# Performance work log

Measured on AMD Instinct MI355X. Metric: run time of the kernel, lower is better.

Reference implementation:

```python
import jax, jax.numpy as jnp
import numpy as np

N = 50000      # total nodes
C = 128        # in_channels
G = 4          # num_groups
B = 50         # number of graphs
NPG = N // B   # nodes per graph = 1000
E = 250000     # total edges (intra-graph)
COUT = 128     # conv out_channels


def setup_inputs() -> dict:
    key = jax.random.key(0)
    ks = jax.random.split(key, 6)
    sc = 1.0 / np.sqrt(C)
    x = jax.random.normal(ks[0], (N, C), dtype=jnp.float32)
    W_group = jax.random.normal(ks[1], (C, G), dtype=jnp.float32) * sc
    W_self = jax.random.normal(ks[2], (C, COUT), dtype=jnp.float32) * sc
    W_nbr = jax.random.normal(ks[3], (C, COUT), dtype=jnp.float32) * sc
    b = jnp.zeros((COUT,), dtype=jnp.float32)
    # intra-graph edges: E//B edges per graph, endpoints offset by graph id
    epg = E // B
    offs = (jnp.arange(E, dtype=jnp.int32) // epg) * NPG
    src = offs + jax.random.randint(ks[4], (E,), 0, NPG, dtype=jnp.int32)
    dst = offs + jax.random.randint(ks[5], (E,), 0, NPG, dtype=jnp.int32)
    edge_index = jnp.stack([src, dst])
    batch = (jnp.arange(N, dtype=jnp.int32) // NPG)
    # expanded node e = i*G*NPG + g*NPG + j maps back to original node i*NPG + j
    eidx = jnp.arange(G * N, dtype=jnp.int32)
    group_ptr = (eidx // (G * NPG)) * NPG + (eidx % NPG)
    return dict(x=x, W_group=W_group, W_self=W_self, W_nbr=W_nbr, b=b,
                edge_index=edge_index, batch=batch, group_ptr=group_ptr)


def reference(x, W_group, W_self, W_nbr, b, edge_index, batch, group_ptr):
    # soft group assignment: s = softmax(x @ W_group).T -> [G, N]
    s = jax.nn.softmax(x @ W_group, axis=-1).T
    # outer-product expansion: [G, N, C]
    ex = s[:, :, None] * x[None, :, :]
    # per-graph cat ordering: (g, graph i, local j) -> i*G*NPG + g*NPG + j
    ex = ex.reshape(G, B, NPG, C).transpose(1, 0, 2, 3).reshape(G * N, C)
    # expanded adjacency: replicate each graph's edges once per group
    src, dst = edge_index[0], edge_index[1]
    goff = jnp.arange(G, dtype=src.dtype)[:, None] * NPG            # [G, 1]
    src_exp = ((src // NPG) * (G * NPG))[None, :] + goff + (src % NPG)[None, :]
    dst_exp = ((dst // NPG) * (G * NPG))[None, :] + goff + (dst % NPG)[None, :]
    src_exp = src_exp.reshape(-1)
    dst_exp = dst_exp.reshape(-1)
    # GraphConv on expanded graph: self transform + sum-aggregated neighbor transform
    msg = (ex @ W_nbr)[src_exp]                                      # [G*E, COUT]
    agg = jax.ops.segment_sum(msg, dst_exp, num_segments=G * N)
    out = ex @ W_self + agg + b                                      # [G*N, COUT]
    # scatter-reduce G group copies back onto N original nodes
    return jax.ops.segment_sum(out, group_ptr, num_segments=N)
```

## Files before the change

kernel.cpp:

```cpp
#include <hip/hip_runtime.h>

constexpr int N_NODES  = 50000;
constexpr int C_IN     = 128;
constexpr int C_OUT    = 128;
constexpr int E_EDGES  = 250000;
constexpr int G_GRP    = 4;
constexpr int TM       = 32;
constexpr int CAP      = 32;
constexpr int NXCD     = 8;


typedef __attribute__((ext_vector_type(8))) short     short8;
typedef __attribute__((ext_vector_type(4))) float     f32x4;
typedef __attribute__((ext_vector_type(2))) unsigned  u32x2;

__device__ __forceinline__ unsigned short f2bf(float f) {
    unsigned u = __builtin_bit_cast(unsigned, f);
    u += 0x7fffu + ((u >> 16) & 1u);
    return (unsigned short)(u >> 16);
}
__device__ __forceinline__ unsigned pack2(float lo, float hi) {
    return (unsigned)f2bf(lo) | ((unsigned)f2bf(hi) << 16);
}

__device__ __forceinline__ int xcd_swizzle(int bid, int nblocks) {
    int q = nblocks / NXCD, r = nblocks % NXCD;
    int xcd = bid % NXCD, lid = bid / NXCD;
    return (xcd < r ? xcd * (q + 1) : r * (q + 1) + (xcd - r) * q) + lid;
}

constexpr int EDGE_BLOCKS  = (E_EDGES + 255) / 256;
constexpr int WPREP_BLOCKS = (C_OUT * 256) / 256;

__global__ __launch_bounds__(256) void fill_prep_kernel(
    const int* __restrict__ src, const int* __restrict__ dst,
    int* __restrict__ cnt, int* __restrict__ buckets,
    const float* __restrict__ Wself, const float* __restrict__ Wnbr,
    unsigned short* __restrict__ WT)
{
    int b = blockIdx.x;
    if (b < EDGE_BLOCKS) {
        int e = b * 256 + threadIdx.x;
        if (e < E_EDGES) {
            int d = dst[e];
            int pos = atomicAdd(&cnt[d], 1);
            if (pos < CAP) buckets[(size_t)d * CAP + pos] = src[e];
        }
    } else {
        int idx = (b - EDGE_BLOCKS) * 256 + threadIdx.x;
        int c = idx >> 8, k = idx & 255;
        float v = (k < 128) ? Wself[k * C_OUT + c] : Wnbr[(k - 128) * C_OUT + c];
        WT[idx] = f2bf(v);
    }
}

constexpr int GATHER_BLOCKS = N_NODES / 8;

__global__ __launch_bounds__(256) void gather_kernel(
    const float* __restrict__ x,
    const int* __restrict__ cnt,
    const int* __restrict__ buckets,
    unsigned short* __restrict__ xa_bf)
{
    int wg   = xcd_swizzle(blockIdx.x, GATHER_BLOCKS);
    int tid  = threadIdx.x;
    int n    = wg * 8 + (tid >> 5);
    int q    = tid & 31;

    const float4* x4 = reinterpret_cast<const float4*>(x);
    int d = cnt[n];
    if (d > CAP) d = CAP;
    const int* sp = buckets + (size_t)n * CAP;

    float ax = 0.f, ay = 0.f, az = 0.f, aw = 0.f;
    int e = 0;
    for (; e + 4 <= d; e += 4) {
        int s0 = sp[e], s1 = sp[e + 1], s2 = sp[e + 2], s3 = sp[e + 3];
        float4 v0 = x4[(size_t)s0 * 32 + q];
        float4 v1 = x4[(size_t)s1 * 32 + q];
        float4 v2 = x4[(size_t)s2 * 32 + q];
        float4 v3 = x4[(size_t)s3 * 32 + q];
        ax += (v0.x + v1.x) + (v2.x + v3.x);
        ay += (v0.y + v1.y) + (v2.y + v3.y);
        az += (v0.z + v1.z) + (v2.z + v3.z);
        aw += (v0.w + v1.w) + (v2.w + v3.w);
    }
    for (; e < d; ++e) {
        int s = sp[e];
        float4 v = x4[(size_t)s * 32 + q];
        ax += v.x; ay += v.y; az += v.z; aw += v.w;
    }

    u32x2 pk{pack2(ax, ay), pack2(az, aw)};
    *reinterpret_cast<u32x2*>(&xa_bf[(size_t)n * 128 + q * 4]) = pk;
}

constexpr int GEMM_BLOCKS = (N_NODES + TM - 1) / TM;

__global__ __launch_bounds__(256) void mfma_gemm_kernel(
    const float* __restrict__ x,
    const unsigned short* __restrict__ xa_bf,
    const unsigned short* __restrict__ WT,
    const float* __restrict__ bias,
    float* __restrict__ out)
{
    __shared__ unsigned char Ab[TM * 512];

    int wg = xcd_swizzle(blockIdx.x, GEMM_BLOCKS);
    const int tid  = threadIdx.x;
    const int row0 = wg * TM;

    #pragma unroll
    for (int i = 0; i < 4; ++i) {
        int idx = tid + i * 256;
        int r = idx >> 5, q = idx & 31;
        int n = row0 + r;
        float4 v = make_float4(0.f, 0.f, 0.f, 0.f);
        if (n < N_NODES) v = reinterpret_cast<const float4*>(x)[(size_t)n * 32 + q];
        unsigned lo = pack2(v.x, v.y), hi = pack2(v.z, v.w);
        int byte = (r * 512 + q * 8) ^ ((r & 7) << 4);
        *reinterpret_cast<u32x2*>(&Ab[byte]) = u32x2{lo, hi};
    }

    #pragma unroll
    for (int i = 0; i < 4; ++i) {
        int idx = tid + i * 256;
        int r = idx >> 5, q = idx & 31;
        int n = row0 + r;
        u32x2 pk{0u, 0u};
        if (n < N_NODES)
            pk = *reinterpret_cast<const u32x2*>(&xa_bf[(size_t)n * 128 + q * 4]);
        int byte = (r * 512 + 256 + q * 8) ^ ((r & 7) << 4);
        *reinterpret_cast<u32x2*>(&Ab[byte]) = pk;
    }
    __syncthreads();

    const int lane = tid & 63;
    const int w    = tid >> 6;
    const int rt   = w >> 1;
    const int ct0  = (w & 1) * 4;

    short8 a[8];
    {
        int r  = rt * 16 + (lane & 15);
        int kb = (lane >> 4) * 16;
        #pragma unroll
        for (int ks = 0; ks < 8; ++ks) {
            int byte = (r * 512 + ks * 64 + kb) ^ ((r & 7) << 4);
            a[ks] = *reinterpret_cast<const short8*>(&Ab[byte]);
        }
    }

    #pragma unroll
    for (int cti = 0; cti < 4; ++cti) {
        int ct = ct0 + cti;
        int c  = ct * 16 + (lane & 15);
        const short8* bp = reinterpret_cast<const short8*>(WT + (size_t)c * 256)
                           + (lane >> 4);
        f32x4 acc = {0.f, 0.f, 0.f, 0.f};
        #pragma unroll
        for (int ks = 0; ks < 8; ++ks) {
            short8 b = bp[ks * 4];
            acc = __builtin_amdgcn_mfma_f32_16x16x32_bf16(a[ks], b, acc, 0, 0, 0);
        }
        float bv = (float)G_GRP * bias[c];
        #pragma unroll
        for (int i = 0; i < 4; ++i) {
            int rr = row0 + rt * 16 + (lane >> 4) * 4 + i;
            if (rr < N_NODES) out[(size_t)rr * C_OUT + c] = acc[i] + bv;
        }
    }
}

extern "C" void kernel_launch(void* const* d_in, const int* in_sizes, int n_in,
                              void* d_out, int out_size, void* d_ws, size_t ws_size,
                              hipStream_t stream)
{
    const float* x     = (const float*)d_in[0];
    const float* Wself = (const float*)d_in[2];
    const float* Wnbr  = (const float*)d_in[3];
    const float* bias  = (const float*)d_in[4];
    const int*   eidx  = (const int*)d_in[5];

    const int* src = eidx;
    const int* dst = eidx + E_EDGES;

    int* cnt     = (int*)d_ws;
    int* buckets = cnt + N_NODES;
    unsigned short* WT    = (unsigned short*)(buckets + (size_t)N_NODES * CAP);
    unsigned short* xa_bf = WT + (size_t)C_OUT * 256;

    float* out = (float*)d_out;

    hipMemsetAsync(cnt, 0, (size_t)N_NODES * sizeof(int), stream);

    fill_prep_kernel<<<EDGE_BLOCKS + WPREP_BLOCKS, 256, 0, stream>>>(
        src, dst, cnt, buckets, Wself, Wnbr, WT);

    gather_kernel<<<GATHER_BLOCKS, 256, 0, stream>>>(x, cnt, buckets, xa_bf);

    mfma_gemm_kernel<<<GEMM_BLOCKS, 256, 0, stream>>>(
        x, xa_bf, WT, bias, out);
}
```

Measured before the change: 67.38 us.

## Replace bucket build and gather with per-graph LDS atomic scatter, enlarge GEMM tiles

```diff
diff --git a/kernel.cpp b/kernel.cpp
--- a/kernel.cpp
+++ b/kernel.cpp
@@ -5,9 +5,9 @@
 constexpr int C_OUT    = 128;
 constexpr int E_EDGES  = 250000;
 constexpr int G_GRP    = 4;
-constexpr int TM       = 32;
-constexpr int CAP      = 32;
-constexpr int NXCD     = 8;
+constexpr int NPG      = 1000;
+constexpr int EPG      = 5000;
+constexpr int B_GRAPHS = 50;
 
 
 typedef __attribute__((ext_vector_type(8))) short     short8;
@@ -23,108 +23,103 @@
     return (unsigned)f2bf(lo) | ((unsigned)f2bf(hi) << 16);
 }
 
-__device__ __forceinline__ int xcd_swizzle(int bid, int nblocks) {
-    int q = nblocks / NXCD, r = nblocks % NXCD;
-    int xcd = bid % NXCD, lid = bid / NXCD;
-    return (xcd < r ? xcd * (q + 1) : r * (q + 1) + (xcd - r) * q) + lid;
-}
+constexpr int SCATTER_BLOCKS = B_GRAPHS * 4;
+constexpr int WPREP_BLOCKS   = (C_OUT * 256) / 512;
 
-constexpr int EDGE_BLOCKS  = (E_EDGES + 255) / 256;
-constexpr int WPREP_BLOCKS = (C_OUT * 256) / 256;
+__global__ __launch_bounds__(512) void scatter_prep_kernel(
+    const float* __restrict__ x,
+    const int* __restrict__ src, const int* __restrict__ dst,
+    const float* __restrict__ Wself, const float* __restrict__ Wnbr,
+    unsigned short* __restrict__ WT, unsigned short* __restrict__ xa_bf)
+{
+    __shared__ float acc[NPG * 32];
 
-__global__ __launch_bounds__(256) void fill_prep_kernel(
-    const int* __restrict__ src, const int* __restrict__ dst,
-    int* __restrict__ cnt, int* __restrict__ buckets,
-    const float* __restrict__ Wself, const float* __restrict__ Wnbr,
-    unsigned short* __restrict__ WT)
-{
-    int b = blockIdx.x;
-    if (b < EDGE_BLOCKS) {
-        int e = b * 256 + threadIdx.x;
-        if (e < E_EDGES) {
-            int d = dst[e];
-            int pos = atomicAdd(&cnt[d], 1);
-            if (pos < CAP) buckets[(size_t)d * CAP + pos] = src[e];
-        }
-    } else {
-        int idx = (b - EDGE_BLOCKS) * 256 + threadIdx.x;
+    const int b   = blockIdx.x;
+    const int tid = threadIdx.x;
+
+    if (b >= SCATTER_BLOCKS) {
+        int idx = (b - SCATTER_BLOCKS) * 512 + tid;
         int c = idx >> 8, k = idx & 255;
         float v = (k < 128) ? Wself[k * C_OUT + c] : Wnbr[(k - 128) * C_OUT + c];
         WT[idx] = f2bf(v);
+        return;
+    }
+
+    const int g   = b >> 2;
+    const int qt  = b & 3;
+    const int ch0 = qt * 32;
+
+    {
+        float4* a4 = reinterpret_cast<float4*>(acc);
+        for (int i = tid; i < NPG * 8; i += 512)
+            a4[i] = make_float4(0.f, 0.f, 0.f, 0.f);
+    }
+    __syncthreads();
+
+    {
+        const int lg = tid >> 5;
+        const int ch = tid & 31;
+        const int eb = g * EPG;
+        const int nb = g * NPG;
+        int i = lg;
+        for (; i + 32 <= EPG; i += 32) {
+            int e0 = eb + i, e1 = eb + i + 16;
+            int s0 = src[e0], d0 = dst[e0];
+            int s1 = src[e1], d1 = dst[e1];
+            float v0 = x[(size_t)s0 * C_IN + ch0 + ch];
+            float v1 = x[(size_t)s1 * C_IN + ch0 + ch];
+            atomicAdd(&acc[(d0 - nb) * 32 + ch], v0);
+            atomicAdd(&acc[(d1 - nb) * 32 + ch], v1);
+        }
+        for (; i < EPG; i += 16) {
+            int e = eb + i;
+            int s = src[e], d = dst[e];
+            float v = x[(size_t)s * C_IN + ch0 + ch];
+            atomicAdd(&acc[(d - nb) * 32 + ch], v);
+        }
+    }
+    __syncthreads();
+
+    {
+        const int lg = tid >> 5;
+        const int ch = tid & 31;
+        const int nb = g * NPG;
+        for (int i = lg; i < NPG; i += 16) {
+            float v = acc[i * 32 + ch];
+            xa_bf[(size_t)(nb + i) * C_IN + ch0 + ch] = f2bf(v);
+        }
     }
 }
 
-constexpr int GATHER_BLOCKS = N_NODES / 8;
+constexpr int TMG         = 256;
+constexpr int GEMM_BLOCKS = (N_NODES + TMG - 1) / TMG;
 
-__global__ __launch_bounds__(256) void gather_kernel(
-    const float* __restrict__ x,
-    const int* __restrict__ cnt,
-    const int* __restrict__ buckets,
-    unsigned short* __restrict__ xa_bf)
-{
-    int wg   = xcd_swizzle(blockIdx.x, GATHER_BLOCKS);
-    int tid  = threadIdx.x;
-    int n    = wg * 8 + (tid >> 5);
-    int q    = tid & 31;
-
-    const float4* x4 = reinterpret_cast<const float4*>(x);
-    int d = cnt[n];
-    if (d > CAP) d = CAP;
-    const int* sp = buckets + (size_t)n * CAP;
-
-    float ax = 0.f, ay = 0.f, az = 0.f, aw = 0.f;
-    int e = 0;
-    for (; e + 4 <= d; e += 4) {
-        int s0 = sp[e], s1 = sp[e + 1], s2 = sp[e + 2], s3 = sp[e + 3];
-        float4 v0 = x4[(size_t)s0 * 32 + q];
-        float4 v1 = x4[(size_t)s1 * 32 + q];
-        float4 v2 = x4[(size_t)s2 * 32 + q];
-        float4 v3 = x4[(size_t)s3 * 32 + q];
-        ax += (v0.x + v1.x) + (v2.x + v3.x);
-        ay += (v0.y + v1.y) + (v2.y + v3.y);
-        az += (v0.z + v1.z) + (v2.z + v3.z);
-        aw += (v0.w + v1.w) + (v2.w + v3.w);
-    }
-    for (; e < d; ++e) {
-        int s = sp[e];
-        float4 v = x4[(size_t)s * 32 + q];
-        ax += v.x; ay += v.y; az += v.z; aw += v.w;
-    }
-
-    u32x2 pk{pack2(ax, ay), pack2(az, aw)};
-    *reinterpret_cast<u32x2*>(&xa_bf[(size_t)n * 128 + q * 4]) = pk;
-}
-
-constexpr int GEMM_BLOCKS = (N_NODES + TM - 1) / TM;
-
-__global__ __launch_bounds__(256) void mfma_gemm_kernel(
+__global__ __launch_bounds__(512, 2) void mfma_gemm_kernel(
     const float* __restrict__ x,
     const unsigned short* __restrict__ xa_bf,
     const unsigned short* __restrict__ WT,
     const float* __restrict__ bias,
     float* __restrict__ out)
 {
-    __shared__ unsigned char Ab[TM * 512];
+    __shared__ unsigned char Ab[TMG * 512];
 
-    int wg = xcd_swizzle(blockIdx.x, GEMM_BLOCKS);
     const int tid  = threadIdx.x;
-    const int row0 = wg * TM;
+    const int row0 = blockIdx.x * TMG;
 
     #pragma unroll
-    for (int i = 0; i < 4; ++i) {
-        int idx = tid + i * 256;
+    for (int i = 0; i < 16; ++i) {
+        int idx = tid + i * 512;
         int r = idx >> 5, q = idx & 31;
         int n = row0 + r;
         float4 v = make_float4(0.f, 0.f, 0.f, 0.f);
         if (n < N_NODES) v = reinterpret_cast<const float4*>(x)[(size_t)n * 32 + q];
-        unsigned lo = pack2(v.x, v.y), hi = pack2(v.z, v.w);
         int byte = (r * 512 + q * 8) ^ ((r & 7) << 4);
-        *reinterpret_cast<u32x2*>(&Ab[byte]) = u32x2{lo, hi};
+        *reinterpret_cast<u32x2*>(&Ab[byte]) = u32x2{pack2(v.x, v.y), pack2(v.z, v.w)};
     }
 
     #pragma unroll
-    for (int i = 0; i < 4; ++i) {
-        int idx = tid + i * 256;
+    for (int i = 0; i < 16; ++i) {
+        int idx = tid + i * 512;
         int r = idx >> 5, q = idx & 31;
         int n = row0 + r;
         u32x2 pk{0u, 0u};
@@ -133,41 +128,48 @@
         int byte = (r * 512 + 256 + q * 8) ^ ((r & 7) << 4);
         *reinterpret_cast<u32x2*>(&Ab[byte]) = pk;
     }
-    __syncthreads();
 
     const int lane = tid & 63;
     const int w    = tid >> 6;
-    const int rt   = w >> 1;
     const int ct0  = (w & 1) * 4;
+    const int rtb  = (w >> 1) * 4;
 
-    short8 a[8];
-    {
+    short8 bfrag[4][8];
+    #pragma unroll
+    for (int cti = 0; cti < 4; ++cti) {
+        int c = (ct0 + cti) * 16 + (lane & 15);
+        const short8* bp = reinterpret_cast<const short8*>(WT + (size_t)c * 256)
+                           + (lane >> 4);
+        #pragma unroll
+        for (int ks = 0; ks < 8; ++ks) bfrag[cti][ks] = bp[ks * 4];
+    }
+    __syncthreads();
+
+    #pragma unroll
+    for (int j = 0; j < 4; ++j) {
+        int rt = rtb + j;
         int r  = rt * 16 + (lane & 15);
         int kb = (lane >> 4) * 16;
+        short8 a[8];
         #pragma unroll
         for (int ks = 0; ks < 8; ++ks) {
             int byte = (r * 512 + ks * 64 + kb) ^ ((r & 7) << 4);
             a[ks] = *reinterpret_cast<const short8*>(&Ab[byte]);
         }
-    }
-
-    #pragma unroll
-    for (int cti = 0; cti < 4; ++cti) {
-        int ct = ct0 + cti;
-        int c  = ct * 16 + (lane & 15);
-        const short8* bp = reinterpret_cast<const short8*>(WT + (size_t)c * 256)
-                           + (lane >> 4);
-        f32x4 acc = {0.f, 0.f, 0.f, 0.f};
         #pragma unroll
-        for (int ks = 0; ks < 8; ++ks) {
-            short8 b = bp[ks * 4];
-            acc = __builtin_amdgcn_mfma_f32_16x16x32_bf16(a[ks], b, acc, 0, 0, 0);
-        }
-        float bv = (float)G_GRP * bias[c];
-        #pragma unroll
-        for (int i = 0; i < 4; ++i) {
-            int rr = row0 + rt * 16 + (lane >> 4) * 4 + i;
-            if (rr < N_NODES) out[(size_t)rr * C_OUT + c] = acc[i] + bv;
+        for (int cti = 0; cti < 4; ++cti) {
+            f32x4 acc = {0.f, 0.f, 0.f, 0.f};
+            #pragma unroll
+            for (int ks = 0; ks < 8; ++ks)
+                acc = __builtin_amdgcn_mfma_f32_16x16x32_bf16(a[ks], bfrag[cti][ks],
+                                                              acc, 0, 0, 0);
+            int c  = (ct0 + cti) * 16 + (lane & 15);
+            float bv = (float)G_GRP * bias[c];
+            #pragma unroll
+            for (int ii = 0; ii < 4; ++ii) {
+                int rr = row0 + rt * 16 + (lane >> 4) * 4 + ii;
+                if (rr < N_NODES) out[(size_t)rr * C_OUT + c] = acc[ii] + bv;
+            }
         }
     }
 }
@@ -185,20 +187,13 @@
     const int* src = eidx;
     const int* dst = eidx + E_EDGES;
 
-    int* cnt     = (int*)d_ws;
-    int* buckets = cnt + N_NODES;
-    unsigned short* WT    = (unsigned short*)(buckets + (size_t)N_NODES * CAP);
+    unsigned short* WT    = (unsigned short*)d_ws;
     unsigned short* xa_bf = WT + (size_t)C_OUT * 256;
 
     float* out = (float*)d_out;
 
-    hipMemsetAsync(cnt, 0, (size_t)N_NODES * sizeof(int), stream);
+    scatter_prep_kernel<<<SCATTER_BLOCKS + WPREP_BLOCKS, 512, 0, stream>>>(
+        x, src, dst, Wself, Wnbr, WT, xa_bf);
 
-    fill_prep_kernel<<<EDGE_BLOCKS + WPREP_BLOCKS, 256, 0, stream>>>(
-        src, dst, cnt, buckets, Wself, Wnbr, WT);
-
-    gather_kernel<<<GATHER_BLOCKS, 256, 0, stream>>>(x, cnt, buckets, xa_bf);
-
-    mfma_gemm_kernel<<<GEMM_BLOCKS, 256, 0, stream>>>(
-        x, xa_bf, WT, bias, out);
+    mfma_gemm_kernel<<<GEMM_BLOCKS, 512, 0, stream>>>(x, xa_bf, WT, bias, out);
 }
```

Measured after the change: 235.9 us. 250% more time.
